# Optimization experiments

Hardware: AMD Instinct MI355X
Metric: run time of the kernel (lower is better)

The kernel has to match this reference:

```python
import jax, jax.numpy as jnp
import numpy as np

N = 16_777_216          # number of probability scores
NUM_BINS = 4096         # calibration bin edges
BIN_MIN, BIN_MAX = -8.0, 8.0
EPS = 1e-3


def setup_inputs() -> dict:
    key = jax.random.key(0)
    Xs = jax.random.uniform(key, (N,), dtype=jnp.float32,
                            minval=EPS, maxval=1.0 - EPS)
    bins = jnp.linspace(BIN_MIN, BIN_MAX, NUM_BINS, dtype=jnp.float32)
    return {"Xs": Xs, "bins": bins}


def reference(Xs, bins):
    # get_scores: log-odds transform
    scores = jnp.log(Xs) - jnp.log(1.0 - Xs)
    # discretize (use_gradients=True path):
    # clamp below first edge, then find j with bins[j] <= s < bins[j] + width[j].
    # Since widths are consecutive-edge differences (last = inf), this is exactly
    # searchsorted(side='right') - 1 on the clamped scores. This replaces the
    # original O(N * num_bins) dense broadcast with a binary search.
    clamped = jnp.maximum(scores, bins[0])
    idx = jnp.searchsorted(bins, clamped, side='right') - 1
    idx = jnp.clip(idx, 0, bins.shape[0] - 1)
    scores_bins = bins[idx]
    # straight-through: forward value = bin edge, gradient flows through scores
    return scores - jax.lax.stop_gradient(scores - scores_bins)
```

## Files before the change

kernel.cpp:

```cpp
#include <hip/hip_runtime.h>

#define NBINS 4096
#define BIN_MIN_F (-8.0f)
#define STEP_F (16.0f / 4095.0f)
#define INV_STEP (4095.0f / 16.0f)
#define LN2_F 0.69314718055994531f

__device__ __forceinline__ float fast_logit(float x) {
    float l0 = __builtin_amdgcn_logf(x);
    float l1 = __builtin_amdgcn_logf(1.0f - x);
    return LN2_F * (l0 - l1);
}

__device__ __forceinline__ float quantize(float s) {
    float c = fmaxf(s, BIN_MIN_F);
    int idx = (int)((c - BIN_MIN_F) * INV_STEP);
    idx = min(max(idx, 0), NBINS - 1);
    return fmaf((float)idx, STEP_F, BIN_MIN_F);
}

__global__ __launch_bounds__(256) void logodds_bins_kernel(
    const float* __restrict__ Xs,
    float* __restrict__ out,
    int n)
{
    const int n4 = n >> 2;
    const int stride = gridDim.x * blockDim.x;

    for (int i = blockIdx.x * blockDim.x + threadIdx.x; i < n4; i += stride) {
        float4 xv = reinterpret_cast<const float4*>(Xs)[i];
        float4 r;
        r.x = quantize(fast_logit(xv.x));
        r.y = quantize(fast_logit(xv.y));
        r.z = quantize(fast_logit(xv.z));
        r.w = quantize(fast_logit(xv.w));
        reinterpret_cast<float4*>(out)[i] = r;
    }

    if (blockIdx.x == 0) {
        int base = n4 << 2;
        for (int t = base + (int)threadIdx.x; t < n; t += blockDim.x) {
            out[t] = quantize(fast_logit(Xs[t]));
        }
    }
}

extern "C" void kernel_launch(void* const* d_in, const int* in_sizes, int n_in,
                              void* d_out, int out_size, void* d_ws, size_t ws_size,
                              hipStream_t stream) {
    const float* Xs = (const float*)d_in[0];
    float* out      = (float*)d_out;
    const int n = in_sizes[0];

    const int block = 256;
    int n4 = n >> 2;
    int grid = (n4 + block - 1) / block;
    if (grid > 2048) grid = 2048;
    if (grid < 1) grid = 1;

    logodds_bins_kernel<<<grid, block, 0, stream>>>(Xs, out, n);
}
```

Baseline: 25.64 us.

## Replace grid-stride loop with batched nontemporal vector loads per thread

Drops the capped grid-stride loop and launches one block per 1024 float4 elements. Each thread issues four independent 16-byte loads up front, then computes and writes them back. Loads and stores use nontemporal builtins to bypass cache retention for streaming data. The aim is more memory-level parallelism per thread and less cache pollution, at the cost of a much larger grid (about 4096 blocks) and more registers per thread.

```diff
diff --git a/kernel.cpp b/kernel.cpp
--- a/kernel.cpp
+++ b/kernel.cpp
@@ -5,6 +5,9 @@
 #define STEP_F (16.0f / 4095.0f)
 #define INV_STEP (4095.0f / 16.0f)
 #define LN2_F 0.69314718055994531f
+#define VEC 4
+
+typedef float f32x4 __attribute__((ext_vector_type(4)));
 
 __device__ __forceinline__ float fast_logit(float x) {
     float l0 = __builtin_amdgcn_logf(x);
@@ -19,27 +22,47 @@
     return fmaf((float)idx, STEP_F, BIN_MIN_F);
 }
 
+__device__ __forceinline__ f32x4 process4(f32x4 xv) {
+    f32x4 r;
+    #pragma unroll
+    for (int j = 0; j < 4; ++j)
+        r[j] = quantize(fast_logit(xv[j]));
+    return r;
+}
+
 __global__ __launch_bounds__(256) void logodds_bins_kernel(
     const float* __restrict__ Xs,
     float* __restrict__ out,
     int n)
 {
     const int n4 = n >> 2;
-    const int stride = gridDim.x * blockDim.x;
+    const f32x4* __restrict__ in4 = reinterpret_cast<const f32x4*>(Xs);
+    f32x4* __restrict__ out4      = reinterpret_cast<f32x4*>(out);
 
-    for (int i = blockIdx.x * blockDim.x + threadIdx.x; i < n4; i += stride) {
-        float4 xv = reinterpret_cast<const float4*>(Xs)[i];
-        float4 r;
-        r.x = quantize(fast_logit(xv.x));
-        r.y = quantize(fast_logit(xv.y));
-        r.z = quantize(fast_logit(xv.z));
-        r.w = quantize(fast_logit(xv.w));
-        reinterpret_cast<float4*>(out)[i] = r;
+    const int base = blockIdx.x * (blockDim.x * VEC) + threadIdx.x;
+
+    int idx[VEC];
+    bool ok[VEC];
+    f32x4 v[VEC];
+
+    #pragma unroll
+    for (int k = 0; k < VEC; ++k) {
+        idx[k] = base + k * 256;
+        ok[k] = idx[k] < n4;
+        if (ok[k]) v[k] = __builtin_nontemporal_load(&in4[idx[k]]);
+    }
+
+    #pragma unroll
+    for (int k = 0; k < VEC; ++k) {
+        if (ok[k]) {
+            f32x4 r = process4(v[k]);
+            __builtin_nontemporal_store(r, &out4[idx[k]]);
+        }
     }
 
     if (blockIdx.x == 0) {
-        int base = n4 << 2;
-        for (int t = base + (int)threadIdx.x; t < n; t += blockDim.x) {
+        int tb = n4 << 2;
+        for (int t = tb + (int)threadIdx.x; t < n; t += blockDim.x) {
             out[t] = quantize(fast_logit(Xs[t]));
         }
     }
@@ -53,9 +76,9 @@
     const int n = in_sizes[0];
 
     const int block = 256;
+    const int per_block = block * VEC;
     int n4 = n >> 2;
-    int grid = (n4 + block - 1) / block;
-    if (grid > 2048) grid = 2048;
+    int grid = (n4 + per_block - 1) / per_block;
     if (grid < 1) grid = 1;
 
     logodds_bins_kernel<<<grid, block, 0, stream>>>(Xs, out, n);
```

Result: slower. 26.50 us (+3.3%).
